# Kernel optimization log

Measured on AMD Instinct MI355X. Metric: run time of the kernel, lower is better.

## Reference

```python
import jax, jax.numpy as jnp
import numpy as np
import math

STEM = 64
TOK = 128
RADIUS = 0.16
K = 32


def sinusoidal_pos_emb_3d(x, dim):
    # x: [..., 3] -> [..., dim]; dim/3 channels per axis (half sin, half cos)
    per_axis = dim // 3
    half = per_axis // 2
    scale = math.log(10000.0) / (half - 1)
    freqs = jnp.exp(-scale * jnp.arange(half, dtype=x.dtype))  # [half]
    ang = x[..., :, None] * freqs  # [..., 3, half]
    emb = jnp.concatenate([jnp.sin(ang), jnp.cos(ang)], axis=-1)  # [..., 3, per_axis]
    return emb.reshape(*x.shape[:-1], dim)


def query_ball_point(radius, nsample, xyz):
    # xyz: [B, N, 3] -> idx [B, N, nsample] int32
    B, N, _ = xyz.shape
    d2 = jnp.sum((xyz[:, :, None, :] - xyz[:, None, :, :]) ** 2, axis=-1)  # [B,N,N]
    cand = jnp.where(d2 <= radius * radius, jnp.arange(N, dtype=jnp.int32)[None, None, :], N)
    idx = jnp.sort(cand, axis=-1)[..., :nsample]  # first nsample in-ball indices
    first = idx[..., :1]  # self is always in-ball (d=0), so first is valid
    return jnp.where(idx == N, first, idx)


def index_points(points, idx):
    # points [B,N,C], idx [B,S,K] -> [B,S,K,C]
    return jax.vmap(lambda p, i: p[i])(points, idx)


def point_mlp(x, W, b, activate):
    y = x @ W + b
    return jax.nn.relu(y) if activate else y


def setup_inputs() -> dict:
    key = jax.random.key(0)
    ks = jax.random.split(key, 10)
    B, N = 2, 4096
    xyz = jax.random.uniform(ks[0], (B, N, 3), dtype=jnp.float32)
    point_feature = jax.random.normal(ks[1], (B, N, STEM), dtype=jnp.float32)
    c_in = STEM + 3 + 24 + 96  # 187
    def lin(k, i, o):
        s = 1.0 / np.sqrt(i)
        return jax.random.uniform(k, (i, o), jnp.float32, -s, s)
    W1 = lin(ks[2], c_in, TOK); b1 = jnp.zeros((TOK,), jnp.float32)
    W2 = lin(ks[3], TOK, TOK); b2 = jnp.zeros((TOK,), jnp.float32)
    W3 = lin(ks[4], TOK, TOK); b3 = jnp.zeros((TOK,), jnp.float32)
    W4 = lin(ks[5], TOK, TOK); b4 = jnp.zeros((TOK,), jnp.float32)
    return {"xyz": xyz, "point_feature": point_feature,
            "W1": W1, "b1": b1, "W2": W2, "b2": b2,
            "W3": W3, "b3": b3, "W4": W4, "b4": b4}


def reference(xyz, point_feature, W1, b1, W2, b2, W3, b3, W4, b4):
    idx = query_ball_point(RADIUS, K, xyz)                 # [B,N,K]
    grouped_xyz = index_points(xyz, idx)                   # [B,N,K,3]
    grouped_feature = index_points(point_feature, idx)     # [B,N,K,STEM]
    relative_xyz = grouped_xyz - xyz[:, :, None, :]        # [B,N,K,3]
    rel_pe = sinusoidal_pos_emb_3d(relative_xyz, 24)       # [B,N,K,24]
    abs_pe = sinusoidal_pos_emb_3d(xyz, 96)                # [B,N,96]
    abs_pe = jnp.broadcast_to(abs_pe[:, :, None, :], (*idx.shape, 96))
    grouped_input = jnp.concatenate(
        [grouped_feature, relative_xyz, rel_pe, abs_pe], axis=-1)  # [B,N,K,187]
    h = point_mlp(grouped_input, W1, b1, True)
    h = point_mlp(h, W2, b2, False)                        # [B,N,K,TOK]
    scene_point_feature = jnp.max(h, axis=2)               # [B,N,TOK]
    g = jnp.max(scene_point_feature, axis=1, keepdims=True)  # [B,1,TOK]
    g = point_mlp(g, W3, b3, True)
    return point_mlp(g, W4, b4, False)                     # [B,1,TOK]
```

## Files before the change

kernel.cpp:

```cpp
#include <hip/hip_runtime.h>
#include <stdint.h>

#define BATCH 2
#define NPTS  4096
#define KNBR  32
#define TOKC  128

typedef _Float16 half8 __attribute__((ext_vector_type(8)));
typedef _Float16 half4 __attribute__((ext_vector_type(4)));
typedef float    f32x4 __attribute__((ext_vector_type(4)));

#define OFF_FH   (1u << 20)
#define OFF_AH   (3u << 20)
#define OFF_GMAX (5u << 20)
#define OFF_W1F  ((5u << 20) + 2048)
#define OFF_W2F  ((5u << 20) + 10240)

__device__ __forceinline__ unsigned int fkey(float f) {
    unsigned int u = __float_as_uint(f);
    return (u & 0x80000000u) ? ~u : (u | 0x80000000u);
}
__device__ __forceinline__ float funkey(unsigned int k) {
    return __uint_as_float((k & 0x80000000u) ? (k ^ 0x80000000u) : ~k);
}

__global__ __launch_bounds__(256) void k_pre(const float* __restrict__ xyz,
                                             const float* __restrict__ W1,
                                             const float* __restrict__ W2,
                                             int* __restrict__ oidx,
                                             _Float16* __restrict__ W1F,
                                             _Float16* __restrict__ W2F,
                                             unsigned int* __restrict__ gmax) {
    const int t = threadIdx.x;
    if (blockIdx.x >= 2048) {
        int f = blockIdx.x - 2048;
        if (f == 0) {
            if (t < 256) gmax[t] = 0u;
            if (t == 0) gmax[256] = 0u;
        }
        #pragma unroll
        for (int s = 0; s < 2; s++) {
            int e = t + s * 256;
            int lane = e >> 3, j = e & 7;
            int l15 = lane & 15, g = lane >> 4;
            if (f < 8) {
                int k = g * 8 + j;
                int c = f * 16 + l15;
                float val = (k < 27) ? W1[(64 + k) * TOKC + c] : 0.f;
                W1F[f * 512 + e] = (_Float16)val;
            } else {
                int f2 = f - 8;
                int ct = f2 >> 2, kc = f2 & 3;
                int k = kc * 32 + g * 8 + j;
                int c = ct * 16 + l15;
                W2F[f2 * 512 + e] = (_Float16)W2[k * TOKC + c];
            }
        }
        return;
    }
    const int w = t >> 6, lane = t & 63;
    int wave = blockIdx.x * 4 + w;
    int b = wave >> 12;
    int n = wave & (NPTS - 1);
    const float* xb = xyz + (size_t)b * NPTS * 3;
    float cx = xb[n * 3 + 0], cy = xb[n * 3 + 1], cz = xb[n * 3 + 2];
    const float R2 = 0.0256f;
    int cnt = 0;
    int first = 0;
    int* out = oidx + (size_t)wave * KNBR;
    float px = xb[lane * 3 + 0], py = xb[lane * 3 + 1], pz = xb[lane * 3 + 2];
    for (int base = 0; base < NPTS; base += 64) {
        #pragma clang fp contract(off)
        float dx = px - cx, dy = py - cy, dz = pz - cz;
        float d2 = (dx * dx + dy * dy) + dz * dz;
        bool hit = d2 <= R2;
        int jn = ((base + 64) & (NPTS - 1)) + lane;
        float nx = xb[jn * 3 + 0], ny = xb[jn * 3 + 1], nz = xb[jn * 3 + 2];
        unsigned long long m = __ballot(hit);
        if (cnt == 0 && m) first = base + (int)__builtin_ctzll(m);
        if (hit) {
            int pos = cnt + (int)__popcll(m & ((1ull << lane) - 1ull));
            if (pos < KNBR) out[pos] = base + lane;
        }
        cnt += (int)__popcll(m);
        if (cnt >= KNBR) break;
        px = nx; py = ny; pz = nz;
    }
    if (lane >= cnt && lane < KNBR) out[lane] = first;
}

__global__ __launch_bounds__(256) void k_prep(const float* __restrict__ xyz,
                                              const float* __restrict__ feat,
                                              const float* __restrict__ W1,
                                              const float* __restrict__ b1,
                                              _Float16* __restrict__ Fh,
                                              _Float16* __restrict__ Ah) {
    __shared__ __align__(16) _Float16 inL[16][168];
    const int t = threadIdx.x;
    const int w = t >> 6, lane = t & 63;
    const int l15 = lane & 15, g = lane >> 4;
    const int g0 = blockIdx.x * 16;

    half8 af[2][2];
    half8 ap[2][3];
    float4 b1v[2];
    #pragma unroll
    for (int rt = 0; rt < 2; rt++) {
        int c = 32 * w + 16 * rt + l15;
        #pragma unroll
        for (int kc = 0; kc < 2; kc++)
            #pragma unroll
            for (int j = 0; j < 8; j++)
                af[rt][kc][j] = (_Float16)W1[(kc * 32 + g * 8 + j) * TOKC + c];
        #pragma unroll
        for (int kc = 0; kc < 3; kc++)
            #pragma unroll
            for (int j = 0; j < 8; j++)
                ap[rt][kc][j] = (_Float16)W1[(91 + kc * 32 + g * 8 + j) * TOKC + c];
        b1v[rt] = *(const float4*)&b1[32 * w + 16 * rt + g * 4];
    }

    {
        float4 v = ((const float4*)(feat + (size_t)g0 * 64))[t];
        half4 hv = {(_Float16)v.x, (_Float16)v.y, (_Float16)v.z, (_Float16)v.w};
        *(half4*)&inL[t >> 4][(t & 15) * 4] = hv;
    }
    {
        int p = t >> 4, v0 = (t & 15) * 6;
        const float* xp = xyz + (size_t)(g0 + p) * 3;
        #pragma unroll
        for (int u = 0; u < 6; u++) {
            int d = v0 + u;
            int a = d >> 5, i = d & 31, fi = i & 15;
            float fr = __expf(-0.6140226914650789f * (float)fi);
            float ang = xp[a] * fr;
            inL[p][64 + d] = (_Float16)((i < 16) ? __sinf(ang) : __cosf(ang));
        }
    }
    __syncthreads();

    f32x4 cF[2], cA[2];
    #pragma unroll
    for (int rt = 0; rt < 2; rt++) { f32x4 z = {0.f, 0.f, 0.f, 0.f}; cF[rt] = z; cA[rt] = z; }
    #pragma unroll
    for (int kc = 0; kc < 2; kc++) {
        half8 bx = *(const half8*)&inL[l15][kc * 32 + g * 8];
        cF[0] = __builtin_amdgcn_mfma_f32_16x16x32_f16(af[0][kc], bx, cF[0], 0, 0, 0);
        cF[1] = __builtin_amdgcn_mfma_f32_16x16x32_f16(af[1][kc], bx, cF[1], 0, 0, 0);
    }
    #pragma unroll
    for (int kc = 0; kc < 3; kc++) {
        half8 bx = *(const half8*)&inL[l15][64 + kc * 32 + g * 8];
        cA[0] = __builtin_amdgcn_mfma_f32_16x16x32_f16(ap[0][kc], bx, cA[0], 0, 0, 0);
        cA[1] = __builtin_amdgcn_mfma_f32_16x16x32_f16(ap[1][kc], bx, cA[1], 0, 0, 0);
    }

    size_t pbase = ((size_t)g0 + l15) * TOKC;
    #pragma unroll
    for (int rt = 0; rt < 2; rt++) {
        int ch0 = 32 * w + 16 * rt + g * 4;
        half4 fv, av;
        #pragma unroll
        for (int r = 0; r < 4; r++) {
            fv[r] = (_Float16)cF[rt][r];
            av[r] = (_Float16)(cA[rt][r] + b1v[rt][r]);
        }
        *(half4*)&Fh[pbase + ch0] = fv;
        *(half4*)&Ah[pbase + ch0] = av;
    }
}

__global__ __launch_bounds__(256, 3) void k_main(const float* __restrict__ xyz,
                                                 const int* __restrict__ idxw,
                                                 const _Float16* __restrict__ Fh,
                                                 const _Float16* __restrict__ Ah,
                                                 const _Float16* __restrict__ W1F,
                                                 const _Float16* __restrict__ W2F,
                                                 unsigned int* __restrict__ gmax,
                                                 const float* __restrict__ b2,
                                                 const float* __restrict__ W3,
                                                 const float* __restrict__ b3,
                                                 const float* __restrict__ W4,
                                                 const float* __restrict__ b4,
                                                 float* __restrict__ outp) {
    __shared__ __align__(16) _Float16 xinL[128 * 40];
    __shared__ __align__(16) _Float16 hfa[128 * 136];
    __shared__ __align__(16) _Float16 arowL[512];
    __shared__ int jidxL[128];
    __shared__ unsigned int lastFlag;

    const int t = threadIdx.x;
    const int w = t >> 6, lane = t & 63;
    const int l15 = lane & 15, g = lane >> 4;
    const int b = blockIdx.x >> 8;
    const int pbase = (blockIdx.x & 255) * 16;
    const float* xb = xyz + (size_t)b * NPTS * 3;

    half8 a1[2];
    half8 a2[2][4];
    #pragma unroll
    for (int rt = 0; rt < 2; rt++) {
        a1[rt] = *(const half8*)&W1F[(2 * w + rt) * 512 + lane * 8];
        #pragma unroll
        for (int kc = 0; kc < 4; kc++)
            a2[rt][kc] = *(const half8*)&W2F[(((2 * w + rt) * 4 + kc)) * 512 + lane * 8];
    }

    float mx[2][4];
    #pragma unroll
    for (int rt = 0; rt < 2; rt++)
        #pragma unroll
        for (int r = 0; r < 4; r++) mx[rt][r] = -1e30f;

    const float FR[4] = {1.f, 0.0464158883f, 0.00215443469f, 1e-4f};

    int jreg = 0;
    ushort ar0, ar1;
    {
        const size_t gq = (size_t)b * NPTS + pbase;
        if (t < 128) jreg = idxw[gq * KNBR + t];
        const ushort* Ain = (const ushort*)(Ah + gq * TOKC);
        ar0 = Ain[t]; ar1 = Ain[t + 256];
    }

    for (int it = 0; it < 4; it++) {
        const int n0 = pbase + it * 4;
        const size_t gp0 = (size_t)b * NPTS + n0;

        if (t < 128) jidxL[t] = jreg;
        ((ushort*)arowL)[t]       = ar0;
        ((ushort*)arowL)[t + 256] = ar1;
        __syncthreads();

        if (it < 3) {
            const size_t gq = gp0 + 4;
            if (t < 128) jreg = idxw[gq * KNBR + t];
            const ushort* Ain = (const ushort*)(Ah + gq * TOKC);
            ar0 = Ain[t]; ar1 = Ain[t + 256];
        }

        {
            int p = t >> 1, hh = t & 1;
            int n = n0 + (p >> 5), j = jidxL[p];
            const half8* frp = (const half8*)(Fh + ((size_t)b * NPTS + j) * TOKC + hh * 64);
            half8 fb[8];
            #pragma unroll
            for (int i = 0; i < 8; i++) fb[i] = frp[i];

            float rx = xb[j * 3 + 0] - xb[n * 3 + 0];
            float ry = xb[j * 3 + 1] - xb[n * 3 + 1];
            float rz = xb[j * 3 + 2] - xb[n * 3 + 2];
            float v[16];
            if (hh == 0) {
                v[0] = rx; v[1] = ry; v[2] = rz;
                #pragma unroll
                for (int fi = 0; fi < 4; fi++) {
                    float ang = rx * FR[fi];
                    v[3 + fi] = __sinf(ang);
                    v[7 + fi] = __cosf(ang);
                }
                #pragma unroll
                for (int fi = 0; fi < 4; fi++) v[11 + fi] = __sinf(ry * FR[fi]);
                v[15] = __cosf(ry * FR[0]);
            } else {
                #pragma unroll
                for (int fi = 1; fi < 4; fi++) v[fi - 1] = __cosf(ry * FR[fi]);
                #pragma unroll
                for (int fi = 0; fi < 4; fi++) {
                    float ang = rz * FR[fi];
                    v[3 + fi] = __sinf(ang);
                    v[7 + fi] = __cosf(ang);
                }
                #pragma unroll
                for (int i = 11; i < 16; i++) v[i] = 0.f;
            }
            half8 h0, h1;
            #pragma unroll
            for (int i = 0; i < 8; i++) { h0[i] = (_Float16)v[i]; h1[i] = (_Float16)v[8 + i]; }
            *(half8*)&xinL[p * 40 + hh * 16]     = h0;
            *(half8*)&xinL[p * 40 + hh * 16 + 8] = h1;

            const half8* arp = (const half8*)(arowL + (p >> 5) * TOKC + hh * 64);
            half8* dst = (half8*)(hfa + p * 136 + hh * 64);
            #pragma unroll
            for (int i = 0; i < 8; i++) dst[i] = fb[i] + arp[i];
        }
        __syncthreads();

        #pragma unroll
        for (int ct = 0; ct < 8; ct++) {
            int p = ct * 16 + l15;
            half8 bx = *(const half8*)&xinL[p * 40 + g * 8];
            f32x4 z = {0.f, 0.f, 0.f, 0.f};
            f32x4 c1a = __builtin_amdgcn_mfma_f32_16x16x32_f16(a1[0], bx, z, 0, 0, 0);
            f32x4 c1b = __builtin_amdgcn_mfma_f32_16x16x32_f16(a1[1], bx, z, 0, 0, 0);
            #pragma unroll
            for (int rt = 0; rt < 2; rt++) {
                int ch0 = 32 * w + 16 * rt + g * 4;
                half4* hp = (half4*)&hfa[p * 136 + ch0];
                half4 bias = *hp;
                f32x4 cc = rt ? c1b : c1a;
                half4 hv;
                #pragma unroll
                for (int r = 0; r < 4; r++) {
                    float s = cc[r] + (float)bias[r];
                    hv[r] = (_Float16)fmaxf(s, 0.f);
                }
                *hp = hv;
            }
        }
        __syncthreads();

        f32x4 c2[8][2];
        #pragma unroll
        for (int ct = 0; ct < 8; ct++)
            #pragma unroll
            for (int rt = 0; rt < 2; rt++) {
                f32x4 z = {0.f, 0.f, 0.f, 0.f};
                c2[ct][rt] = z;
            }
        #pragma unroll
        for (int kc = 0; kc < 4; kc++) {
            #pragma unroll
            for (int ct = 0; ct < 8; ct++) {
                half8 bx = *(const half8*)&hfa[(ct * 16 + l15) * 136 + kc * 32 + g * 8];
                c2[ct][0] = __builtin_amdgcn_mfma_f32_16x16x32_f16(a2[0][kc], bx, c2[ct][0], 0, 0, 0);
                c2[ct][1] = __builtin_amdgcn_mfma_f32_16x16x32_f16(a2[1][kc], bx, c2[ct][1], 0, 0, 0);
            }
        }
        #pragma unroll
        for (int ct = 0; ct < 8; ct++)
            #pragma unroll
            for (int rt = 0; rt < 2; rt++)
                #pragma unroll
                for (int r = 0; r < 4; r++)
                    mx[rt][r] = fmaxf(mx[rt][r], c2[ct][rt][r]);
        __syncthreads();
    }

    #pragma unroll
    for (int rt = 0; rt < 2; rt++)
        #pragma unroll
        for (int r = 0; r < 4; r++) {
            float v = mx[rt][r];
            #pragma unroll
            for (int off = 1; off < 16; off <<= 1)
                v = fmaxf(v, __shfl_xor(v, off));
            if (l15 == 0) {
                int ch = 32 * w + 16 * rt + g * 4 + r;
                atomicMax(&gmax[b * TOKC + ch], fkey(v));
            }
        }

    if (t == 0) {
        __threadfence();
        unsigned int v = atomicAdd(&gmax[256], 1u);
        lastFlag = (v == 511u) ? 1u : 0u;
    }
    __syncthreads();
    if (lastFlag) {
        float* gl = (float*)xinL;
        float* sl = gl + 256;
        int bb = t >> 7, c = t & 127;
        unsigned int key = atomicOr(&gmax[bb * TOKC + c], 0u);
        gl[t] = funkey(key) + b2[c];
        __syncthreads();
        float s = b3[c];
        for (int k = 0; k < 128; k++) s += gl[bb * 128 + k] * W3[k * TOKC + c];
        sl[t] = fmaxf(s, 0.f);
        __syncthreads();
        float o = b4[c];
        for (int k = 0; k < 128; k++) o += sl[bb * 128 + k] * W4[k * TOKC + c];
        outp[t] = o;
    }
}

extern "C" void kernel_launch(void* const* d_in, const int* in_sizes, int n_in,
                              void* d_out, int out_size, void* d_ws, size_t ws_size,
                              hipStream_t stream) {
    const float* xyz  = (const float*)d_in[0];
    const float* feat = (const float*)d_in[1];
    const float* W1   = (const float*)d_in[2];
    const float* b1   = (const float*)d_in[3];
    const float* W2   = (const float*)d_in[4];
    const float* b2   = (const float*)d_in[5];
    const float* W3   = (const float*)d_in[6];
    const float* b3   = (const float*)d_in[7];
    const float* W4   = (const float*)d_in[8];
    const float* b4   = (const float*)d_in[9];

    char* ws = (char*)d_ws;
    int*          idxw = (int*)ws;
    _Float16*     Fh   = (_Float16*)(ws + OFF_FH);
    _Float16*     Ah   = (_Float16*)(ws + OFF_AH);
    unsigned int* gmax = (unsigned int*)(ws + OFF_GMAX);
    _Float16*     W1F  = (_Float16*)(ws + OFF_W1F);
    _Float16*     W2F  = (_Float16*)(ws + OFF_W2F);

    k_pre<<<dim3(2088), dim3(256), 0, stream>>>(xyz, W1, W2, idxw, W1F, W2F, gmax);
    k_prep<<<dim3((BATCH * NPTS) / 16), dim3(256), 0, stream>>>(xyz, feat, W1, b1, Fh, Ah);
    k_main<<<dim3(512), dim3(256), 0, stream>>>(xyz, idxw, Fh, Ah, W1F, W2F, gmax,
                                                b2, W3, b3, W4, b4, (float*)d_out);
}
```

Baseline: 147.7 us.

## Merge prep kernels and split main kernel into many small two-point blocks

Folds k_prep into k_pre as extra block ranges, so one fewer kernel launch is needed. k_main now handles 2 points (64 neighbour rows) per block across 4096 blocks instead of looping over 16 points in 512 blocks. It halves shared memory, raises launch bounds occupancy to 6, and drops the software prefetch loop. The aim is more parallelism and latency hiding on the MI355X, at the cost of more per-block overhead, reloading W1F/W2F fragments in every block, and 8x more global atomics on gmax.

```diff
diff --git a/kernel.cpp b/kernel.cpp
--- a/kernel.cpp
+++ b/kernel.cpp
@@ -16,6 +16,8 @@
 #define OFF_W1F  ((5u << 20) + 2048)
 #define OFF_W2F  ((5u << 20) + 10240)
 
+#define NMAIN 4096
+
 __device__ __forceinline__ unsigned int fkey(float f) {
     unsigned int u = __float_as_uint(f);
     return (u & 0x80000000u) ? ~u : (u | 0x80000000u);
@@ -25,15 +27,54 @@
 }
 
 __global__ __launch_bounds__(256) void k_pre(const float* __restrict__ xyz,
+                                             const float* __restrict__ feat,
                                              const float* __restrict__ W1,
                                              const float* __restrict__ W2,
+                                             const float* __restrict__ b1,
                                              int* __restrict__ oidx,
+                                             _Float16* __restrict__ Fh,
+                                             _Float16* __restrict__ Ah,
                                              _Float16* __restrict__ W1F,
                                              _Float16* __restrict__ W2F,
                                              unsigned int* __restrict__ gmax) {
+    __shared__ __align__(16) _Float16 inL[16][168];
     const int t = threadIdx.x;
-    if (blockIdx.x >= 2048) {
-        int f = blockIdx.x - 2048;
+    const int w = t >> 6, lane = t & 63;
+
+    if (blockIdx.x < 2048) {
+        int wave = blockIdx.x * 4 + w;
+        int b = wave >> 12;
+        int n = wave & (NPTS - 1);
+        const float* xb = xyz + (size_t)b * NPTS * 3;
+        float cx = xb[n * 3 + 0], cy = xb[n * 3 + 1], cz = xb[n * 3 + 2];
+        const float R2 = 0.0256f;
+        int cnt = 0;
+        int first = 0;
+        int* out = oidx + (size_t)wave * KNBR;
+        float px = xb[lane * 3 + 0], py = xb[lane * 3 + 1], pz = xb[lane * 3 + 2];
+        for (int base = 0; base < NPTS; base += 64) {
+            #pragma clang fp contract(off)
+            float dx = px - cx, dy = py - cy, dz = pz - cz;
+            float d2 = (dx * dx + dy * dy) + dz * dz;
+            bool hit = d2 <= R2;
+            int jn = ((base + 64) & (NPTS - 1)) + lane;
+            float nx = xb[jn * 3 + 0], ny = xb[jn * 3 + 1], nz = xb[jn * 3 + 2];
+            unsigned long long m = __ballot(hit);
+            if (cnt == 0 && m) first = base + (int)__builtin_ctzll(m);
+            if (hit) {
+                int pos = cnt + (int)__popcll(m & ((1ull << lane) - 1ull));
+                if (pos < KNBR) out[pos] = base + lane;
+            }
+            cnt += (int)__popcll(m);
+            if (cnt >= KNBR) break;
+            px = nx; py = ny; pz = nz;
+        }
+        if (lane >= cnt && lane < KNBR) out[lane] = first;
+        return;
+    }
+
+    if (blockIdx.x >= 2560) {
+        int f = blockIdx.x - 2560;
         if (f == 0) {
             if (t < 256) gmax[t] = 0u;
             if (t == 0) gmax[256] = 0u;
@@ -41,8 +82,8 @@
         #pragma unroll
         for (int s = 0; s < 2; s++) {
             int e = t + s * 256;
-            int lane = e >> 3, j = e & 7;
-            int l15 = lane & 15, g = lane >> 4;
+            int ln = e >> 3, j = e & 7;
+            int l15 = ln & 15, g = ln >> 4;
             if (f < 8) {
                 int k = g * 8 + j;
                 int c = f * 16 + l15;
@@ -58,48 +99,9 @@
         }
         return;
     }
-    const int w = t >> 6, lane = t & 63;
-    int wave = blockIdx.x * 4 + w;
-    int b = wave >> 12;
-    int n = wave & (NPTS - 1);
-    const float* xb = xyz + (size_t)b * NPTS * 3;
-    float cx = xb[n * 3 + 0], cy = xb[n * 3 + 1], cz = xb[n * 3 + 2];
-    const float R2 = 0.0256f;
-    int cnt = 0;
-    int first = 0;
-    int* out = oidx + (size_t)wave * KNBR;
-    float px = xb[lane * 3 + 0], py = xb[lane * 3 + 1], pz = xb[lane * 3 + 2];
-    for (int base = 0; base < NPTS; base += 64) {
-        #pragma clang fp contract(off)
-        float dx = px - cx, dy = py - cy, dz = pz - cz;
-        float d2 = (dx * dx + dy * dy) + dz * dz;
-        bool hit = d2 <= R2;
-        int jn = ((base + 64) & (NPTS - 1)) + lane;
-        float nx = xb[jn * 3 + 0], ny = xb[jn * 3 + 1], nz = xb[jn * 3 + 2];
-        unsigned long long m = __ballot(hit);
-        if (cnt == 0 && m) first = base + (int)__builtin_ctzll(m);
-        if (hit) {
-            int pos = cnt + (int)__popcll(m & ((1ull << lane) - 1ull));
-            if (pos < KNBR) out[pos] = base + lane;
-        }
-        cnt += (int)__popcll(m);
-        if (cnt >= KNBR) break;
-        px = nx; py = ny; pz = nz;
-    }
-    if (lane >= cnt && lane < KNBR) out[lane] = first;
-}
-
-__global__ __launch_bounds__(256) void k_prep(const float* __restrict__ xyz,
-                                              const float* __restrict__ feat,
-                                              const float* __restrict__ W1,
-                                              const float* __restrict__ b1,
-                                              _Float16* __restrict__ Fh,
-                                              _Float16* __restrict__ Ah) {
-    __shared__ __align__(16) _Float16 inL[16][168];
-    const int t = threadIdx.x;
-    const int w = t >> 6, lane = t & 63;
+
     const int l15 = lane & 15, g = lane >> 4;
-    const int g0 = blockIdx.x * 16;
+    const int g0 = (blockIdx.x - 2048) * 16;
 
     half8 af[2][2];
     half8 ap[2][3];
@@ -170,7 +172,7 @@
     }
 }
 
-__global__ __launch_bounds__(256, 3) void k_main(const float* __restrict__ xyz,
+__global__ __launch_bounds__(256, 6) void k_main(const float* __restrict__ xyz,
                                                  const int* __restrict__ idxw,
                                                  const _Float16* __restrict__ Fh,
                                                  const _Float16* __restrict__ Ah,
@@ -183,17 +185,18 @@
                                                  const float* __restrict__ W4,
                                                  const float* __restrict__ b4,
                                                  float* __restrict__ outp) {
-    __shared__ __align__(16) _Float16 xinL[128 * 40];
-    __shared__ __align__(16) _Float16 hfa[128 * 136];
-    __shared__ __align__(16) _Float16 arowL[512];
-    __shared__ int jidxL[128];
+    __shared__ __align__(16) _Float16 xinL[64 * 40];
+    __shared__ __align__(16) _Float16 hfa[64 * 136];
+    __shared__ __align__(16) _Float16 arowL[256];
+    __shared__ int jidxL[64];
     __shared__ unsigned int lastFlag;
 
     const int t = threadIdx.x;
     const int w = t >> 6, lane = t & 63;
     const int l15 = lane & 15, g = lane >> 4;
-    const int b = blockIdx.x >> 8;
-    const int pbase = (blockIdx.x & 255) * 16;
+    const int b = blockIdx.x >> 11;
+    const int n0 = (blockIdx.x & 2047) * 2;
+    const size_t gp0 = (size_t)b * NPTS + n0;
     const float* xb = xyz + (size_t)b * NPTS * 3;
 
     half8 a1[2];
@@ -203,140 +206,111 @@
         a1[rt] = *(const half8*)&W1F[(2 * w + rt) * 512 + lane * 8];
         #pragma unroll
         for (int kc = 0; kc < 4; kc++)
-            a2[rt][kc] = *(const half8*)&W2F[(((2 * w + rt) * 4 + kc)) * 512 + lane * 8];
-    }
-
+            a2[rt][kc] = *(const half8*)&W2F[((2 * w + rt) * 4 + kc) * 512 + lane * 8];
+    }
+
+    if (t < 64) jidxL[t] = idxw[gp0 * KNBR + t];
+    ((ushort*)arowL)[t] = ((const ushort*)(Ah + gp0 * TOKC))[t];
+    __syncthreads();
+
+    const float FR[4] = {1.f, 0.0464158883f, 0.00215443469f, 1e-4f};
+    {
+        int p = t >> 2, q = t & 3;
+        int j = jidxL[p];
+        const half8* frp = (const half8*)(Fh + ((size_t)b * NPTS + j) * TOKC + q * 32);
+        half8 fb[4];
+        #pragma unroll
+        for (int i = 0; i < 4; i++) fb[i] = frp[i];
+        const half8* arp = (const half8*)(arowL + (p >> 5) * TOKC + q * 32);
+        half8* dst = (half8*)(hfa + p * 136 + q * 32);
+        #pragma unroll
+        for (int i = 0; i < 4; i++) dst[i] = fb[i] + arp[i];
+    }
+    if (t < 128) {
+        int p = t >> 1, hh = t & 1;
+        int n = n0 + (p >> 5), j = jidxL[p];
+        float rx = xb[j * 3 + 0] - xb[n * 3 + 0];
+        float ry = xb[j * 3 + 1] - xb[n * 3 + 1];
+        float rz = xb[j * 3 + 2] - xb[n * 3 + 2];
+        float v[16];
+        if (hh == 0) {
+            v[0] = rx; v[1] = ry; v[2] = rz;
+            #pragma unroll
+            for (int fi = 0; fi < 4; fi++) {
+                float ang = rx * FR[fi];
+                v[3 + fi] = __sinf(ang);
+                v[7 + fi] = __cosf(ang);
+            }
+            #pragma unroll
+            for (int fi = 0; fi < 4; fi++) v[11 + fi] = __sinf(ry * FR[fi]);
+            v[15] = __cosf(ry * FR[0]);
+        } else {
+            #pragma unroll
+            for (int fi = 1; fi < 4; fi++) v[fi - 1] = __cosf(ry * FR[fi]);
+            #pragma unroll
+            for (int fi = 0; fi < 4; fi++) {
+                float ang = rz * FR[fi];
+                v[3 + fi] = __sinf(ang);
+                v[7 + fi] = __cosf(ang);
+            }
+            #pragma unroll
+            for (int i = 11; i < 16; i++) v[i] = 0.f;
+        }
+        half8 h0, h1;
+        #pragma unroll
+        for (int i = 0; i < 8; i++) { h0[i] = (_Float16)v[i]; h1[i] = (_Float16)v[8 + i]; }
+        *(half8*)&xinL[p * 40 + hh * 16]     = h0;
+        *(half8*)&xinL[p * 40 + hh * 16 + 8] = h1;
+    }
+    __syncthreads();
+
+    #pragma unroll
+    for (int ct = 0; ct < 4; ct++) {
+        int p = ct * 16 + l15;
+        half8 bx = *(const half8*)&xinL[p * 40 + g * 8];
+        f32x4 z = {0.f, 0.f, 0.f, 0.f};
+        f32x4 c1a = __builtin_amdgcn_mfma_f32_16x16x32_f16(a1[0], bx, z, 0, 0, 0);
+        f32x4 c1b = __builtin_amdgcn_mfma_f32_16x16x32_f16(a1[1], bx, z, 0, 0, 0);
+        #pragma unroll
+        for (int rt = 0; rt < 2; rt++) {
+            int ch0 = 32 * w + 16 * rt + g * 4;
+            half4* hp = (half4*)&hfa[p * 136 + ch0];
+            half4 bias = *hp;
+            f32x4 cc = rt ? c1b : c1a;
+            half4 hv;
+            #pragma unroll
+            for (int r = 0; r < 4; r++) {
+                float s = cc[r] + (float)bias[r];
+                hv[r] = (_Float16)fmaxf(s, 0.f);
+            }
+            *hp = hv;
+        }
+    }
+    __syncthreads();
+
+    f32x4 c2[4][2];
+    #pragma unroll
+    for (int ct = 0; ct < 4; ct++)
+        #pragma unroll
+        for (int rt = 0; rt < 2; rt++) {
+            f32x4 z = {0.f, 0.f, 0.f, 0.f};
+            c2[ct][rt] = z;
+        }
+    #pragma unroll
+    for (int kc = 0; kc < 4; kc++) {
+        #pragma unroll
+        for (int ct = 0; ct < 4; ct++) {
+            half8 bx = *(const half8*)&hfa[(ct * 16 + l15) * 136 + kc * 32 + g * 8];
+            c2[ct][0] = __builtin_amdgcn_mfma_f32_16x16x32_f16(a2[0][kc], bx, c2[ct][0], 0, 0, 0);
+            c2[ct][1] = __builtin_amdgcn_mfma_f32_16x16x32_f16(a2[1][kc], bx, c2[ct][1], 0, 0, 0);
+        }
+    }
     float mx[2][4];
     #pragma unroll
     for (int rt = 0; rt < 2; rt++)
         #pragma unroll
-        for (int r = 0; r < 4; r++) mx[rt][r] = -1e30f;
-
-    const float FR[4] = {1.f, 0.0464158883f, 0.00215443469f, 1e-4f};
-
-    int jreg = 0;
-    ushort ar0, ar1;
-    {
-        const size_t gq = (size_t)b * NPTS + pbase;
-        if (t < 128) jreg = idxw[gq * KNBR + t];
-        const ushort* Ain = (const ushort*)(Ah + gq * TOKC);
-        ar0 = Ain[t]; ar1 = Ain[t + 256];
-    }
-
-    for (int it = 0; it < 4; it++) {
-        const int n0 = pbase + it * 4;
-        const size_t gp0 = (size_t)b * NPTS + n0;
-
-        if (t < 128) jidxL[t] = jreg;
-        ((ushort*)arowL)[t]       = ar0;
-        ((ushort*)arowL)[t + 256] = ar1;
-        __syncthreads();
-
-        if (it < 3) {
-            const size_t gq = gp0 + 4;
-            if (t < 128) jreg = idxw[gq * KNBR + t];
-            const ushort* Ain = (const ushort*)(Ah + gq * TOKC);
-            ar0 = Ain[t]; ar1 = Ain[t + 256];
-        }
-
-        {
-            int p = t >> 1, hh = t & 1;
-            int n = n0 + (p >> 5), j = jidxL[p];
-            const half8* frp = (const half8*)(Fh + ((size_t)b * NPTS + j) * TOKC + hh * 64);
-            half8 fb[8];
-            #pragma unroll
-            for (int i = 0; i < 8; i++) fb[i] = frp[i];
-
-            float rx = xb[j * 3 + 0] - xb[n * 3 + 0];
-            float ry = xb[j * 3 + 1] - xb[n * 3 + 1];
-            float rz = xb[j * 3 + 2] - xb[n * 3 + 2];
-            float v[16];
-            if (hh == 0) {
-                v[0] = rx; v[1] = ry; v[2] = rz;
-                #pragma unroll
-                for (int fi = 0; fi < 4; fi++) {
-                    float ang = rx * FR[fi];
-                    v[3 + fi] = __sinf(ang);
-                    v[7 + fi] = __cosf(ang);
-                }
-                #pragma unroll
-                for (int fi = 0; fi < 4; fi++) v[11 + fi] = __sinf(ry * FR[fi]);
-                v[15] = __cosf(ry * FR[0]);
-            } else {
-                #pragma unroll
-                for (int fi = 1; fi < 4; fi++) v[fi - 1] = __cosf(ry * FR[fi]);
-                #pragma unroll
-                for (int fi = 0; fi < 4; fi++) {
-                    float ang = rz * FR[fi];
-                    v[3 + fi] = __sinf(ang);
-                    v[7 + fi] = __cosf(ang);
-                }
-                #pragma unroll
-                for (int i = 11; i < 16; i++) v[i] = 0.f;
-            }
-            half8 h0, h1;
-            #pragma unroll
-            for (int i = 0; i < 8; i++) { h0[i] = (_Float16)v[i]; h1[i] = (_Float16)v[8 + i]; }
-            *(half8*)&xinL[p * 40 + hh * 16]     = h0;
-            *(half8*)&xinL[p * 40 + hh * 16 + 8] = h1;
-
-            const half8* arp = (const half8*)(arowL + (p >> 5) * TOKC + hh * 64);
-            half8* dst = (half8*)(hfa + p * 136 + hh * 64);
-            #pragma unroll
-            for (int i = 0; i < 8; i++) dst[i] = fb[i] + arp[i];
-        }
-        __syncthreads();
-
-        #pragma unroll
-        for (int ct = 0; ct < 8; ct++) {
-            int p = ct * 16 + l15;
-            half8 bx = *(const half8*)&xinL[p * 40 + g * 8];
-            f32x4 z = {0.f, 0.f, 0.f, 0.f};
-            f32x4 c1a = __builtin_amdgcn_mfma_f32_16x16x32_f16(a1[0], bx, z, 0, 0, 0);
-            f32x4 c1b = __builtin_amdgcn_mfma_f32_16x16x32_f16(a1[1], bx, z, 0, 0, 0);
-            #pragma unroll
-            for (int rt = 0; rt < 2; rt++) {
-                int ch0 = 32 * w + 16 * rt + g * 4;
-                half4* hp = (half4*)&hfa[p * 136 + ch0];
-                half4 bias = *hp;
-                f32x4 cc = rt ? c1b : c1a;
-                half4 hv;
-                #pragma unroll
-                for (int r = 0; r < 4; r++) {
-                    float s = cc[r] + (float)bias[r];
-                    hv[r] = (_Float16)fmaxf(s, 0.f);
-                }
-                *hp = hv;
-            }
-        }
-        __syncthreads();
-
-        f32x4 c2[8][2];
-        #pragma unroll
-        for (int ct = 0; ct < 8; ct++)
-            #pragma unroll
-            for (int rt = 0; rt < 2; rt++) {
-                f32x4 z = {0.f, 0.f, 0.f, 0.f};
-                c2[ct][rt] = z;
-            }
-        #pragma unroll
-        for (int kc = 0; kc < 4; kc++) {
-            #pragma unroll
-            for (int ct = 0; ct < 8; ct++) {
-                half8 bx = *(const half8*)&hfa[(ct * 16 + l15) * 136 + kc * 32 + g * 8];
-                c2[ct][0] = __builtin_amdgcn_mfma_f32_16x16x32_f16(a2[0][kc], bx, c2[ct][0], 0, 0, 0);
-                c2[ct][1] = __builtin_amdgcn_mfma_f32_16x16x32_f16(a2[1][kc], bx, c2[ct][1], 0, 0, 0);
-            }
-        }
-        #pragma unroll
-        for (int ct = 0; ct < 8; ct++)
-            #pragma unroll
-            for (int rt = 0; rt < 2; rt++)
-                #pragma unroll
-                for (int r = 0; r < 4; r++)
-                    mx[rt][r] = fmaxf(mx[rt][r], c2[ct][rt][r]);
-        __syncthreads();
-    }
+        for (int r = 0; r < 4; r++)
+            mx[rt][r] = fmaxf(fmaxf(c2[0][rt][r], c2[1][rt][r]), fmaxf(c2[2][rt][r], c2[3][rt][r]));
 
     #pragma unroll
     for (int rt = 0; rt < 2; rt++)
@@ -355,7 +329,7 @@
     if (t == 0) {
         __threadfence();
         unsigned int v = atomicAdd(&gmax[256], 1u);
-        lastFlag = (v == 511u) ? 1u : 0u;
+        lastFlag = (v == (unsigned int)(NMAIN - 1)) ? 1u : 0u;
     }
     __syncthreads();
     if (lastFlag) {
@@ -397,8 +371,8 @@
     _Float16*     W1F  = (_Float16*)(ws + OFF_W1F);
     _Float16*     W2F  = (_Float16*)(ws + OFF_W2F);
 
-    k_pre<<<dim3(2088), dim3(256), 0, stream>>>(xyz, W1, W2, idxw, W1F, W2F, gmax);
-    k_prep<<<dim3((BATCH * NPTS) / 16), dim3(256), 0, stream>>>(xyz, feat, W1, b1, Fh, Ah);
-    k_main<<<dim3(512), dim3(256), 0, stream>>>(xyz, idxw, Fh, Ah, W1F, W2F, gmax,
-                                                b2, W3, b3, W4, b4, (float*)d_out);
-}
+    k_pre<<<dim3(2600), dim3(256), 0, stream>>>(xyz, feat, W1, W2, b1,
+                                                idxw, Fh, Ah, W1F, W2F, gmax);
+    k_main<<<dim3(NMAIN), dim3(256), 0, stream>>>(xyz, idxw, Fh, Ah, W1F, W2F, gmax,
+                                                  b2, W3, b3, W4, b4, (float*)d_out);
+}
```

New measurement: 383.3 us. 159% more time.
